# Kernel tuning notes

Measured on AMD Instinct MI355X. Metric: run time of the kernel, lower is better.

Reference implementation:

```python
import jax, jax.numpy as jnp
import numpy as np

H = 2048  # hidden_size
I = 2048  # input_size
B = 2048  # batch


def setup_inputs() -> dict:
    key = jax.random.key(0)
    k0, k1, k2, k3, k4, k5 = jax.random.split(key, 6)
    # bipolar-domain activations live in [-1, 1]
    inp = jax.random.uniform(k0, (B, I), jnp.float32, minval=-1.0, maxval=1.0)
    hx = jax.random.uniform(k1, (B, H), jnp.float32, minval=-1.0, maxval=1.0)
    s = 1.0 / np.sqrt(H + I)
    w_f = jax.random.normal(k2, (H, H + I), jnp.float32) * s
    b_f = jax.random.normal(k3, (H,), jnp.float32) * s
    w_n = jax.random.normal(k4, (H, H + I), jnp.float32) * s
    b_n = jax.random.normal(k5, (H,), jnp.float32) * s
    return {"input": inp, "hx": hx, "w_f": w_f, "b_f": b_f, "w_n": w_n, "b_n": b_n}


def reference(input, hx, w_f, b_f, w_n, b_n):
    # Expected-value (probability-domain) math of the unary bitstream MGU cell.
    # fg_ug_tanh: FSULinear on [hx, x]; 'hardtanh is direct pass' -> identity act.
    fg_ug_in = jnp.concatenate([hx, input], axis=1)            # [B, H+I]
    fg_in = fg_ug_in @ w_f.T + b_f                              # [B, H]
    # fg_sigmoid: FSUAdd of [fg_in, ones] with scale=None -> (x + 1) / 2
    fg = (fg_in + 1.0) * 0.5                                    # [B, H]
    # fg_hx_mul: FSUMul with static in_1_prob = hx buffer
    fg_hx = fg * hx                                             # [B, H]
    # ng_ug_tanh: FSULinear on [fg*hx, x]
    ng_ug_in = jnp.concatenate([fg_hx, input], axis=1)          # [B, H+I]
    ng = ng_ug_in @ w_n.T + b_n                                 # [B, H]
    # fg_ng_mul: dynamic FSUMul; bipolar bit-inversion (1 - bitstream) negates value
    fg_ng = fg * ng
    # hy_add: FSUAdd([ng, -fg*ng, fg*hx], scale=1) -> plain sum
    hy = ng - fg_ng + fg_hx                                     # = (1-fg)*ng + fg*hx
    return hy
```

## Files before the change

### kernel.cpp

```cpp
#include <hip/hip_runtime.h>
#include <stdint.h>


#define Hdim 2048
#define Idim 2048
#define Bdim 2048
#define Ktot 4096
#define KHALF 2048
#define NSTEP (KHALF / 64)

typedef __bf16 bf16;
typedef __bf16 bf16x8 __attribute__((ext_vector_type(8)));
typedef float  f32x4  __attribute__((ext_vector_type(4)));

__device__ __forceinline__ void gload_lds16(const bf16* g, bf16* l) {
  __builtin_amdgcn_global_load_lds(
      (const __attribute__((address_space(1))) unsigned int*)g,
      (__attribute__((address_space(3))) unsigned int*)l,
      16, 0, 0);
}

__global__ void cvt_kernel(const float* __restrict__ src, bf16* __restrict__ dst, int n8) {
  int stride = gridDim.x * blockDim.x;
  for (int i = blockIdx.x * blockDim.x + threadIdx.x; i < n8; i += stride) {
    const float4* s = (const float4*)src + (size_t)i * 2;
    float4 a = s[0], b = s[1];
    bf16x8 o;
    o[0]=(bf16)a.x; o[1]=(bf16)a.y; o[2]=(bf16)a.z; o[3]=(bf16)a.w;
    o[4]=(bf16)b.x; o[5]=(bf16)b.y; o[6]=(bf16)b.z; o[7]=(bf16)b.w;
    *((bf16x8*)dst + i) = o;
  }
}

__global__ void build_a_kernel(const float* __restrict__ hx, const float* __restrict__ x,
                               bf16* __restrict__ A1, bf16* __restrict__ A2) {
  int stride = gridDim.x * blockDim.x;
  const int n8 = Bdim * Ktot / 8;
  for (int i = blockIdx.x * blockDim.x + threadIdx.x; i < n8; i += stride) {
    int e = i * 8;
    int b = e >> 12;
    int k = e & (Ktot - 1);
    const float* src = (k < Hdim) ? (hx + (size_t)b * Hdim + k)
                                  : (x  + (size_t)b * Idim + (k - Hdim));
    const float4* s = (const float4*)src;
    float4 va = s[0], vb = s[1];
    bf16x8 o;
    o[0]=(bf16)va.x; o[1]=(bf16)va.y; o[2]=(bf16)va.z; o[3]=(bf16)va.w;
    o[4]=(bf16)vb.x; o[5]=(bf16)vb.y; o[6]=(bf16)vb.z; o[7]=(bf16)vb.w;
    *((bf16x8*)A1 + i) = o;
    if (k >= Hdim) *((bf16x8*)A2 + i) = o;
  }
}

template<int EPI>
__global__ __launch_bounds__(512)
void gemm_kernel(const bf16* __restrict__ A, const bf16* __restrict__ W,
                 const float* __restrict__ bias,
                 const float* __restrict__ hx,
                 float* __restrict__ FG,
                 bf16* __restrict__ A2,
                 float* __restrict__ OUT)
{
  __shared__ bf16 lds[2][2][2][8192];

  int bid  = blockIdx.x;
  int sbid = (bid & 7) * 32 + (bid >> 3);
  int tm = sbid >> 4, tn = sbid & 15;

  int tid  = threadIdx.x;
  int w = tid >> 6, lane = tid & 63;
  int g = w >> 2, sub = w & 3;
  int wrow = (sub >> 1) * 64;
  int wcol = (sub & 1) * 64;
  int fr = lane & 15, fq = lane >> 4;
  int swz = fr & 7;

  int gtid = sub * 64 + lane;
  int srow = gtid >> 3;
  int csrc = (gtid & 7) ^ (srow & 7);
  const bf16* pA = A + (size_t)(tm * 128 + srow) * Ktot + csrc * 8 + g * KHALF;
  const bf16* pB = W + (size_t)(tn * 128 + srow) * Ktot + csrc * 8 + g * KHALF;
  int lbase = sub * 512;

#define STAGE(buf, koff) do {                                                      \
    _Pragma("unroll")                                                              \
    for (int j = 0; j < 4; ++j) {                                                  \
      gload_lds16(pA + (size_t)j * 32 * Ktot + (koff), &lds[g][buf][0][j * 2048 + lbase]); \
      gload_lds16(pB + (size_t)j * 32 * Ktot + (koff), &lds[g][buf][1][j * 2048 + lbase]); \
    }                                                                              \
  } while (0)

  f32x4 acc[4][4] = {};

  STAGE(0, 0);
  asm volatile("s_waitcnt vmcnt(0)" ::: "memory");
  __builtin_amdgcn_s_barrier();

  int cur = 0;
  for (int t = 0; t < NSTEP; ++t) {
    const bool pf = (t + 1 < NSTEP);
    #pragma unroll
    for (int kk = 0; kk < 2; ++kk) {
      bf16x8 af[4], bv[4];
      int ch = ((kk * 4 + fq) ^ swz) * 8;
      #pragma unroll
      for (int m = 0; m < 4; ++m)
        af[m] = *(const bf16x8*)&lds[g][cur][0][(wrow + m * 16 + fr) * 64 + ch];
      #pragma unroll
      for (int n = 0; n < 4; ++n)
        bv[n] = *(const bf16x8*)&lds[g][cur][1][(wcol + n * 16 + fr) * 64 + ch];
      if (kk == 0 && pf) STAGE(cur ^ 1, (t + 1) * 64);
      __builtin_amdgcn_sched_barrier(0);
      __builtin_amdgcn_s_barrier();
      __builtin_amdgcn_s_setprio(1);
      #pragma unroll
      for (int m = 0; m < 4; ++m)
        #pragma unroll
        for (int n = 0; n < 4; ++n)
          acc[m][n] = __builtin_amdgcn_mfma_f32_16x16x32_bf16(af[m], bv[n], acc[m][n], 0, 0, 0);
      __builtin_amdgcn_s_setprio(0);
      if (kk == 1 && pf)
        asm volatile("s_waitcnt vmcnt(0)" ::: "memory");
      __builtin_amdgcn_sched_barrier(0);
      __builtin_amdgcn_s_barrier();
    }
    cur ^= 1;
  }
#undef STAGE

  __syncthreads();
  float* xch = (float*)&lds[0][0][0][0];
  if (g == 1) {
    #pragma unroll
    for (int m = 0; m < 4; ++m)
      #pragma unroll
      for (int n = 0; n < 4; ++n)
        *(f32x4*)&xch[sub * 4096 + (m * 4 + n) * 256 + lane * 4] = acc[m][n];
  }
  __syncthreads();
  if (g == 0) {
    int row0 = tm * 128 + wrow + fq * 4;
    int col0 = tn * 128 + wcol + fr;
    #pragma unroll
    for (int n = 0; n < 4; ++n) {
      int gcol = col0 + n * 16;
      float bv = bias[gcol];
      #pragma unroll
      for (int m = 0; m < 4; ++m) {
        f32x4 part = *(const f32x4*)&xch[sub * 4096 + (m * 4 + n) * 256 + lane * 4];
        #pragma unroll
        for (int i = 0; i < 4; ++i) {
          int grow = row0 + m * 16 + i;
          size_t idx = (size_t)grow * Hdim + gcol;
          float v = acc[m][n][i] + part[i] + bv;
          if (EPI == 0) {
            float fg   = (v + 1.0f) * 0.5f;
            float fghx = fg * hx[idx];
            FG[idx] = fg;
            A2[(size_t)grow * Ktot + gcol] = (bf16)fghx;
          } else {
            float fg   = FG[idx];
            float fghx = (float)A2[(size_t)grow * Ktot + gcol];
            OUT[idx] = v - fg * v + fghx;
          }
        }
      }
    }
  }
}

extern "C" void kernel_launch(void* const* d_in, const int* in_sizes, int n_in,
                              void* d_out, int out_size, void* d_ws, size_t ws_size,
                              hipStream_t stream) {
  const float* x   = (const float*)d_in[0];
  const float* hx  = (const float*)d_in[1];
  const float* w_f = (const float*)d_in[2];
  const float* b_f = (const float*)d_in[3];
  const float* w_n = (const float*)d_in[4];
  const float* b_n = (const float*)d_in[5];
  float* out = (float*)d_out;

  bf16* A1 = (bf16*)d_ws;
  bf16* A2 = A1 + (size_t)Bdim * Ktot;
  bf16* Wf = A2 + (size_t)Bdim * Ktot;
  bf16* Wn = Wf + (size_t)Hdim * Ktot;

  const int n8w = Hdim * Ktot / 8;
  cvt_kernel<<<1024, 256, 0, stream>>>(w_f, Wf, n8w);
  cvt_kernel<<<1024, 256, 0, stream>>>(w_n, Wn, n8w);
  build_a_kernel<<<1024, 256, 0, stream>>>(hx, x, A1, A2);

  gemm_kernel<0><<<256, 512, 0, stream>>>(A1, Wf, b_f, hx, out, A2, nullptr);
  gemm_kernel<1><<<256, 512, 0, stream>>>(A2, Wn, b_n, nullptr, out, A2, out);
}
```

Before: 120.8 us.

## Stagger split-K wave groups by one half-step to ping-pong MFMA and memory phases

Reworks the GEMM main loop so that the two split-K wave groups run offset by one half-iteration over 2*NSTEP+1 windows, with one barrier per window instead of two per half-step. While one group issues LDS reads and global->LDS prefetch, the other runs its MFMA block, aiming to overlap memory and matrix work across groups. The change adds an extra window and divergent control flow, and the correctness of the barrier and waitcnt placement depends on the stagger.

```diff
diff --git a/kernel.cpp b/kernel.cpp
--- a/kernel.cpp
+++ b/kernel.cpp
@@ -84,34 +84,42 @@
 
 #define STAGE(buf, koff) do {                                                      \
     _Pragma("unroll")                                                              \
-    for (int j = 0; j < 4; ++j) {                                                  \
-      gload_lds16(pA + (size_t)j * 32 * Ktot + (koff), &lds[g][buf][0][j * 2048 + lbase]); \
-      gload_lds16(pB + (size_t)j * 32 * Ktot + (koff), &lds[g][buf][1][j * 2048 + lbase]); \
+    for (int jj = 0; jj < 4; ++jj) {                                               \
+      gload_lds16(pA + (size_t)jj * 32 * Ktot + (koff), &lds[g][buf][0][jj * 2048 + lbase]); \
+      gload_lds16(pB + (size_t)jj * 32 * Ktot + (koff), &lds[g][buf][1][jj * 2048 + lbase]); \
     }                                                                              \
+  } while (0)
+
+#define READS(buf_, j_) do {                                                       \
+    int ch = (((j_) * 4 + fq) ^ swz) * 8;                                          \
+    _Pragma("unroll")                                                              \
+    for (int m = 0; m < 4; ++m)                                                    \
+      af[m] = *(const bf16x8*)&lds[g][buf_][0][(wrow + m * 16 + fr) * 64 + ch];    \
+    _Pragma("unroll")                                                              \
+    for (int n = 0; n < 4; ++n)                                                    \
+      bv[n] = *(const bf16x8*)&lds[g][buf_][1][(wcol + n * 16 + fr) * 64 + ch];    \
   } while (0)
 
   f32x4 acc[4][4] = {};
 
   STAGE(0, 0);
-  asm volatile("s_waitcnt vmcnt(0)" ::: "memory");
-  __builtin_amdgcn_s_barrier();
 
-  int cur = 0;
-  for (int t = 0; t < NSTEP; ++t) {
-    const bool pf = (t + 1 < NSTEP);
-    #pragma unroll
-    for (int kk = 0; kk < 2; ++kk) {
-      bf16x8 af[4], bv[4];
-      int ch = ((kk * 4 + fq) ^ swz) * 8;
-      #pragma unroll
-      for (int m = 0; m < 4; ++m)
-        af[m] = *(const bf16x8*)&lds[g][cur][0][(wrow + m * 16 + fr) * 64 + ch];
-      #pragma unroll
-      for (int n = 0; n < 4; ++n)
-        bv[n] = *(const bf16x8*)&lds[g][cur][1][(wcol + n * 16 + fr) * 64 + ch];
-      if (kk == 0 && pf) STAGE(cur ^ 1, (t + 1) * 64);
-      __builtin_amdgcn_sched_barrier(0);
-      __builtin_amdgcn_s_barrier();
+  const int NW = 2 * NSTEP + 1;
+  for (int win = 0; win < NW; ++win) {
+    int w2 = win - g;
+    bool active = (unsigned)w2 < (unsigned)(2 * NSTEP);
+    int t = w2 >> 1, j = w2 & 1, buf = t & 1;
+    bf16x8 af[4], bv[4];
+    if (active) {
+      if (j == 1) READS(buf, 1);
+      else asm volatile("s_waitcnt vmcnt(0)" ::: "memory");
+    }
+    __builtin_amdgcn_s_barrier();
+    if (active) {
+      if (j == 0) {
+        READS(buf, 0);
+        if (t + 1 < NSTEP) STAGE(buf ^ 1, (t + 1) * 64);
+      }
       __builtin_amdgcn_s_setprio(1);
       #pragma unroll
       for (int m = 0; m < 4; ++m)
@@ -119,14 +127,10 @@
         for (int n = 0; n < 4; ++n)
           acc[m][n] = __builtin_amdgcn_mfma_f32_16x16x32_bf16(af[m], bv[n], acc[m][n], 0, 0, 0);
       __builtin_amdgcn_s_setprio(0);
-      if (kk == 1 && pf)
-        asm volatile("s_waitcnt vmcnt(0)" ::: "memory");
-      __builtin_amdgcn_sched_barrier(0);
-      __builtin_amdgcn_s_barrier();
     }
-    cur ^= 1;
   }
 #undef STAGE
+#undef READS
 
   __syncthreads();
   float* xch = (float*)&lds[0][0][0][0];
```

Result: faster. 117.9 us (-2.4%).
